# Kernel optimization log

Hardware: AMD Instinct MI355X
Metric: run time of the kernel (lower is better)

Reference implementation:

```python
import jax, jax.numpy as jnp
import numpy as np

B, C, N, M = 128, 1024, 8192, 128  # batch, controller_size, memory_units, key_size(=memory_unit_size)
EPS = 1e-16


def setup_inputs() -> dict:
    key = jax.random.key(0)
    ks = jax.random.split(key, 16)
    controller_state = jax.random.normal(ks[0], (B, C), dtype=jnp.float32)
    pw = jax.random.uniform(ks[1], (B, N), dtype=jnp.float32)
    prev_weights = pw / jnp.sum(pw, axis=1, keepdims=True)  # valid attention distribution
    memory = jax.random.normal(ks[2], (B, N, M), dtype=jnp.float32)
    sc = 0.02
    params = {
        "Wk": sc * jax.random.normal(ks[3], (C, M), dtype=jnp.float32), "bk": jnp.zeros((M,), jnp.float32),
        "Wb": sc * jax.random.normal(ks[4], (C, 1), dtype=jnp.float32), "bb": jnp.zeros((1,), jnp.float32),
        "Wg": sc * jax.random.normal(ks[5], (C, 1), dtype=jnp.float32), "bg": jnp.zeros((1,), jnp.float32),
        "Ws": sc * jax.random.normal(ks[6], (C, 3), dtype=jnp.float32), "bs": jnp.zeros((3,), jnp.float32),
        "Wy": sc * jax.random.normal(ks[7], (C, 1), dtype=jnp.float32), "by": jnp.zeros((1,), jnp.float32),
        "Wa": sc * jax.random.normal(ks[8], (C, M), dtype=jnp.float32), "ba": jnp.zeros((M,), jnp.float32),
    }
    return {"controller_state": controller_state, "prev_weights": prev_weights, "memory": memory, **params}


def reference(controller_state, prev_weights, memory, Wk, bk, Wb, bb, Wg, bg, Ws, bs, Wy, by, Wa, ba):
    cs = controller_state
    k = cs @ Wk + bk                                    # (B, M) key
    beta = jax.nn.softplus(cs @ Wb + bb)                # (B, 1) key strength
    g = jax.nn.sigmoid(cs @ Wg + bg)                    # (B, 1) interpolation gate
    s = jax.nn.softmax(cs @ Ws + bs, axis=1)            # (B, 3) shift weighting
    y = 1.0 + jax.nn.softplus(cs @ Wy + by)             # (B, 1) sharpen factor
    # content addressing: softmax(beta * cosine_sim(key, memory rows))
    dots = jnp.einsum("bnm,bm->bn", memory, k)          # (B, N)
    mnorm = jnp.linalg.norm(memory, axis=2)             # (B, N)
    knorm = jnp.linalg.norm(k, axis=1, keepdims=True)   # (B, 1)
    cos = dots / (mnorm * knorm + EPS)
    content_weights = jax.nn.softmax(beta * cos, axis=1)
    # interpolate with previous weights
    iw = g * content_weights + (1.0 - g) * prev_weights
    # circular 3-tap shift: c[i] = s0*w[i-1] + s1*w[i] + s2*w[i+1] (circular)
    sw = (s[:, 0:1] * jnp.roll(iw, 1, axis=1)
          + s[:, 1:2] * iw
          + s[:, 2:3] * jnp.roll(iw, -1, axis=1))
    # sharpen + normalize
    w = sw ** y
    w = w / (jnp.sum(w, axis=1, keepdims=True) + EPS)
    # read mode: data = w @ memory
    data = jnp.einsum("bn,bnm->bm", w, memory)          # (B, M)
    return (w, data)
```

## Files before the change

kernel.cpp:

```cpp
#include <hip/hip_runtime.h>
#include <math.h>

#define Bsz 128
#define Csz 1024
#define Nsz 8192
#define Msz 128
#define EPSF 1e-16f

__device__ __forceinline__ float softplusf(float x) {
    return (x > 20.f) ? x : log1pf(expf(x));
}

__global__ __launch_bounds__(256) void kA(
    const float* __restrict__ cs,
    const float* __restrict__ Wk, const float* __restrict__ bk,
    const float* __restrict__ Wb, const float* __restrict__ bb,
    const float* __restrict__ Wg, const float* __restrict__ bg,
    const float* __restrict__ Ws, const float* __restrict__ bs,
    const float* __restrict__ Wy, const float* __restrict__ by,
    float* __restrict__ K, float* __restrict__ scal)
{
    const int b = blockIdx.x;
    const int t = threadIdx.x;
    const int m = t & 127, h = t >> 7;
    __shared__ float lcs[Csz];
    __shared__ float kpart[256];
    __shared__ float red[256];

    #pragma unroll
    for (int j = 0; j < Csz / 256; ++j) lcs[t + j * 256] = cs[b * Csz + t + j * 256];
    __syncthreads();

    float ka = 0.f;
    const int c0 = h * (Csz / 2);
    #pragma unroll 8
    for (int c = c0; c < c0 + Csz / 2; ++c) ka += lcs[c] * Wk[c * Msz + m];
    kpart[t] = ka;

    float ab = 0.f, ag = 0.f, ay = 0.f, a0 = 0.f, a1 = 0.f, a2 = 0.f;
    for (int c = t; c < Csz; c += 256) {
        float v = lcs[c];
        ab += v * Wb[c];
        ag += v * Wg[c];
        ay += v * Wy[c];
        a0 += v * Ws[c * 3 + 0];
        a1 += v * Ws[c * 3 + 1];
        a2 += v * Ws[c * 3 + 2];
    }
    __syncthreads();

    float kfull = 0.f;
    if (h == 0) {
        kfull = kpart[m] + kpart[128 + m] + bk[m];
        K[b * Msz + m] = kfull;
    }

    auto redu = [&](float v) -> float {
        __syncthreads();
        red[t] = v;
        __syncthreads();
        for (int off = 128; off > 0; off >>= 1) {
            if (t < off) red[t] += red[t + off];
            __syncthreads();
        }
        return red[0];
    };

    float db = redu(ab);
    float dg = redu(ag);
    float dy = redu(ay);
    float d0 = redu(a0);
    float d1 = redu(a1);
    float d2 = redu(a2);
    float dq = redu(kfull * kfull);

    if (t == 0) {
        float beta = softplusf(db + bb[0]);
        float g = 1.f / (1.f + expf(-(dg + bg[0])));
        float yv = 1.f + softplusf(dy + by[0]);
        float l0 = d0 + bs[0], l1 = d1 + bs[1], l2 = d2 + bs[2];
        float m3 = fmaxf(l0, fmaxf(l1, l2));
        float e0 = expf(l0 - m3), e1 = expf(l1 - m3), e2 = expf(l2 - m3);
        float inv = 1.f / (e0 + e1 + e2);
        scal[b * 8 + 0] = sqrtf(dq);
        scal[b * 8 + 1] = beta;
        scal[b * 8 + 2] = g;
        scal[b * 8 + 3] = e0 * inv;
        scal[b * 8 + 4] = e1 * inv;
        scal[b * 8 + 5] = e2 * inv;
        scal[b * 8 + 6] = yv;
    }
}

__global__ __launch_bounds__(256) void kB(
    const float* __restrict__ mem, const float* __restrict__ K,
    const float* __restrict__ scal, float* __restrict__ z,
    float* __restrict__ sumexp)
{
    const int b = blockIdx.x >> 7;
    const int n0 = (blockIdx.x & 127) * 64;
    const int t = threadIdx.x;
    const int rl = t & 15, rg = t >> 4;

    __shared__ float lk[Msz];
    __shared__ float lred[16];
    if (t < Msz) lk[t] = K[b * Msz + t];
    __syncthreads();

    const float knorm = scal[b * 8 + 0];
    const float beta = scal[b * 8 + 1];

    const float k0 = lk[rl * 4 + 0], k1 = lk[rl * 4 + 1];
    const float k2 = lk[rl * 4 + 2], k3 = lk[rl * 4 + 3];
    const float k4 = lk[64 + rl * 4 + 0], k5 = lk[64 + rl * 4 + 1];
    const float k6 = lk[64 + rl * 4 + 2], k7 = lk[64 + rl * 4 + 3];

    const float* base = mem + (size_t)b * Nsz * Msz;

    float ez = 0.f;
    #pragma unroll
    for (int i = 0; i < 4; ++i) {
        const int n = n0 + i * 16 + rg;
        const float4* p = (const float4*)(base + (size_t)n * Msz);
        float4 a = p[rl];
        float4 c = p[16 + rl];
        float dot = a.x * k0 + a.y * k1 + a.z * k2 + a.w * k3
                  + c.x * k4 + c.y * k5 + c.z * k6 + c.w * k7;
        float sq = a.x * a.x + a.y * a.y + a.z * a.z + a.w * a.w
                 + c.x * c.x + c.y * c.y + c.z * c.z + c.w * c.w;
        #pragma unroll
        for (int off = 8; off; off >>= 1) {
            dot += __shfl_xor(dot, off, 16);
            sq  += __shfl_xor(sq,  off, 16);
        }
        if (rl == 0) {
            float mn = sqrtf(sq);
            float zv = beta * (dot / (mn * knorm + EPSF));
            z[(size_t)b * Nsz + n] = zv;
            ez += expf(zv);
        }
    }
    if (rl == 0) lred[rg] = ez;
    __syncthreads();
    if (t == 0) {
        float s = 0.f;
        #pragma unroll
        for (int j = 0; j < 16; ++j) s += lred[j];
        atomicAdd(&sumexp[b], s);
    }
}

__global__ __launch_bounds__(256) void kD(
    const float* __restrict__ z, const float* __restrict__ pw,
    const float* __restrict__ scal, const float* __restrict__ sumexp,
    float* __restrict__ tbuf, float* __restrict__ S)
{
    const int gid = blockIdx.x * 256 + threadIdx.x;
    const int b = gid >> 13;
    const int n = gid & (Nsz - 1);

    const float invl = 1.f / sumexp[b];
    const float g = scal[b * 8 + 2];
    const float s0 = scal[b * 8 + 3], s1 = scal[b * 8 + 4], s2 = scal[b * 8 + 5];
    const float yv = scal[b * 8 + 6];

    const int nm1 = (n == 0) ? Nsz - 1 : n - 1;
    const int np1 = (n == Nsz - 1) ? 0 : n + 1;
    const size_t bo = (size_t)b * Nsz;

    const float om = 1.f - g;
    float iwm = g * (expf(z[bo + nm1]) * invl) + om * pw[bo + nm1];
    float iw0 = g * (expf(z[bo + n  ]) * invl) + om * pw[bo + n  ];
    float iwp = g * (expf(z[bo + np1]) * invl) + om * pw[bo + np1];

    float sw = s0 * iwm + s1 * iw0 + s2 * iwp;
    float tv = expf(yv * logf(sw));
    tbuf[bo + n] = tv;

    __shared__ float red[256];
    red[threadIdx.x] = tv;
    __syncthreads();
    for (int off = 128; off; off >>= 1) {
        if (threadIdx.x < off) red[threadIdx.x] += red[threadIdx.x + off];
        __syncthreads();
    }
    if (threadIdx.x == 0) atomicAdd(&S[b], red[0]);
}

__global__ __launch_bounds__(256) void kE(
    const float* __restrict__ mem, const float* __restrict__ tbuf,
    const float* __restrict__ S, float* __restrict__ wout,
    float* __restrict__ dacc)
{
    const int ridx = (int)gridDim.x - 1 - (int)blockIdx.x;
    const int b = ridx >> 6;
    const int n0 = (ridx & 63) * 128;
    const int t = threadIdx.x;
    const int rl = t & 15, rg = t >> 4;

    const float invS = 1.f / (S[b] + EPSF);
    const float* base = mem + (size_t)b * Nsz * Msz;
    const float* tb = tbuf + (size_t)b * Nsz;

    float acc[8] = {0.f, 0.f, 0.f, 0.f, 0.f, 0.f, 0.f, 0.f};

    #pragma unroll
    for (int i = 0; i < 8; ++i) {
        const int n = n0 + i * 16 + rg;
        const float tv = tb[n];
        const float4* p = (const float4*)(base + (size_t)n * Msz);
        float4 a = p[rl];
        float4 c = p[16 + rl];
        acc[0] += tv * a.x; acc[1] += tv * a.y; acc[2] += tv * a.z; acc[3] += tv * a.w;
        acc[4] += tv * c.x; acc[5] += tv * c.y; acc[6] += tv * c.z; acc[7] += tv * c.w;
        if (rl == 0) wout[(size_t)b * Nsz + n] = tv * invS;
    }

    __shared__ float red[256 * 8];
    #pragma unroll
    for (int j = 0; j < 8; ++j) red[t * 8 + j] = acc[j];
    __syncthreads();

    if (t < Msz) {
        const int half = t >> 6, rl2 = (t & 63) >> 2, jj = t & 3;
        float s = 0.f;
        #pragma unroll
        for (int gq = 0; gq < 16; ++gq) s += red[(gq * 16 + rl2) * 8 + half * 4 + jj];
        atomicAdd(&dacc[b * Msz + t], s);
    }
}

__global__ __launch_bounds__(256) void kF(
    const float* __restrict__ dacc, const float* __restrict__ S,
    float* __restrict__ dout)
{
    const int gid = blockIdx.x * 256 + threadIdx.x;
    if (gid < Bsz * Msz) {
        const int b = gid >> 7;
        dout[gid] = dacc[gid] / (S[b] + EPSF);
    }
}

extern "C" void kernel_launch(void* const* d_in, const int* in_sizes, int n_in,
                              void* d_out, int out_size, void* d_ws, size_t ws_size,
                              hipStream_t stream) {
    const float* cs  = (const float*)d_in[0];
    const float* pw  = (const float*)d_in[1];
    const float* mem = (const float*)d_in[2];
    const float* Wk  = (const float*)d_in[3];
    const float* bk  = (const float*)d_in[4];
    const float* Wb  = (const float*)d_in[5];
    const float* bb  = (const float*)d_in[6];
    const float* Wg  = (const float*)d_in[7];
    const float* bg  = (const float*)d_in[8];
    const float* Ws  = (const float*)d_in[9];
    const float* bs  = (const float*)d_in[10];
    const float* Wy  = (const float*)d_in[11];
    const float* by  = (const float*)d_in[12];

    float* out = (float*)d_out;
    float* wout = out;
    float* dout = out + (size_t)Bsz * Nsz;

    float* wsf    = (float*)d_ws;
    float* K      = wsf;
    float* scal   = K + Bsz * Msz;
    float* S      = scal + Bsz * 8;
    float* sumexp = S + Bsz;
    float* dacc   = sumexp + Bsz;
    float* z      = dacc + Bsz * Msz;
    float* tbuf   = z + (size_t)Bsz * Nsz;

    hipMemsetAsync(S, 0, (size_t)(Bsz + Bsz + Bsz * Msz) * sizeof(float), stream);

    kA<<<Bsz, 256, 0, stream>>>(cs, Wk, bk, Wb, bb, Wg, bg, Ws, bs, Wy, by, K, scal);
    kB<<<Bsz * (Nsz / 64), 256, 0, stream>>>(mem, K, scal, z, sumexp);
    kD<<<(Bsz * Nsz) / 256, 256, 0, stream>>>(z, pw, scal, sumexp, tbuf, S);
    kE<<<Bsz * (Nsz / 128), 256, 0, stream>>>(mem, tbuf, S, wout, dacc);
    kF<<<(Bsz * Msz + 255) / 256, 256, 0, stream>>>(dacc, S, dout);
}
```

Before: 871.2 us.

## Process batch in chunks so memory re-read hits the last-level cache

Splits the content-addressing, weighting and read kernels into four sequential batch chunks, so the memory slice read by the dot-product kernel is likely still in the large last-level cache when the read kernel touches it again. This targets the second full pass over the large memory tensor from HBM. It adds extra kernel launches and smaller grids per launch, and it replaces the earlier reverse-block-order trick. It also splits the key projection loop into four independent accumulators.

```diff
diff --git a/kernel.cpp b/kernel.cpp
--- a/kernel.cpp
+++ b/kernel.cpp
@@ -6,6 +6,7 @@
 #define Nsz 8192
 #define Msz 128
 #define EPSF 1e-16f
+#define CHUNK 32
 
 __device__ __forceinline__ float softplusf(float x) {
     return (x > 20.f) ? x : log1pf(expf(x));
@@ -31,11 +32,16 @@
     for (int j = 0; j < Csz / 256; ++j) lcs[t + j * 256] = cs[b * Csz + t + j * 256];
     __syncthreads();
 
-    float ka = 0.f;
+    float ka0 = 0.f, ka1 = 0.f, ka2 = 0.f, ka3 = 0.f;
     const int c0 = h * (Csz / 2);
-    #pragma unroll 8
-    for (int c = c0; c < c0 + Csz / 2; ++c) ka += lcs[c] * Wk[c * Msz + m];
-    kpart[t] = ka;
+    #pragma unroll 4
+    for (int c = c0; c < c0 + Csz / 2; c += 4) {
+        ka0 += lcs[c + 0] * Wk[(c + 0) * Msz + m];
+        ka1 += lcs[c + 1] * Wk[(c + 1) * Msz + m];
+        ka2 += lcs[c + 2] * Wk[(c + 2) * Msz + m];
+        ka3 += lcs[c + 3] * Wk[(c + 3) * Msz + m];
+    }
+    kpart[t] = (ka0 + ka1) + (ka2 + ka3);
 
     float ab = 0.f, ag = 0.f, ay = 0.f, a0 = 0.f, a1 = 0.f, a2 = 0.f;
     for (int c = t; c < Csz; c += 256) {
@@ -95,9 +101,9 @@
 __global__ __launch_bounds__(256) void kB(
     const float* __restrict__ mem, const float* __restrict__ K,
     const float* __restrict__ scal, float* __restrict__ z,
-    float* __restrict__ sumexp)
-{
-    const int b = blockIdx.x >> 7;
+    float* __restrict__ sumexp, int b0)
+{
+    const int b = b0 + (blockIdx.x >> 7);
     const int n0 = (blockIdx.x & 127) * 64;
     const int t = threadIdx.x;
     const int rl = t & 15, rg = t >> 4;
@@ -153,10 +159,10 @@
 __global__ __launch_bounds__(256) void kD(
     const float* __restrict__ z, const float* __restrict__ pw,
     const float* __restrict__ scal, const float* __restrict__ sumexp,
-    float* __restrict__ tbuf, float* __restrict__ S)
+    float* __restrict__ tbuf, float* __restrict__ S, int b0)
 {
     const int gid = blockIdx.x * 256 + threadIdx.x;
-    const int b = gid >> 13;
+    const int b = b0 + (gid >> 13);
     const int n = gid & (Nsz - 1);
 
     const float invl = 1.f / sumexp[b];
@@ -190,11 +196,10 @@
 __global__ __launch_bounds__(256) void kE(
     const float* __restrict__ mem, const float* __restrict__ tbuf,
     const float* __restrict__ S, float* __restrict__ wout,
-    float* __restrict__ dacc)
-{
-    const int ridx = (int)gridDim.x - 1 - (int)blockIdx.x;
-    const int b = ridx >> 6;
-    const int n0 = (ridx & 63) * 128;
+    float* __restrict__ dacc, int b0)
+{
+    const int b = b0 + (blockIdx.x >> 6);
+    const int n0 = (blockIdx.x & 63) * 128;
     const int t = threadIdx.x;
     const int rl = t & 15, rg = t >> 4;
 
@@ -274,8 +279,13 @@
     hipMemsetAsync(S, 0, (size_t)(Bsz + Bsz + Bsz * Msz) * sizeof(float), stream);
 
     kA<<<Bsz, 256, 0, stream>>>(cs, Wk, bk, Wb, bb, Wg, bg, Ws, bs, Wy, by, K, scal);
-    kB<<<Bsz * (Nsz / 64), 256, 0, stream>>>(mem, K, scal, z, sumexp);
-    kD<<<(Bsz * Nsz) / 256, 256, 0, stream>>>(z, pw, scal, sumexp, tbuf, S);
-    kE<<<Bsz * (Nsz / 128), 256, 0, stream>>>(mem, tbuf, S, wout, dacc);
+
+    for (int c = Bsz / CHUNK - 1; c >= 0; --c) {
+        const int b0 = c * CHUNK;
+        kB<<<CHUNK * (Nsz / 64), 256, 0, stream>>>(mem, K, scal, z, sumexp, b0);
+        kD<<<(CHUNK * Nsz) / 256, 256, 0, stream>>>(z, pw, scal, sumexp, tbuf, S, b0);
+        kE<<<CHUNK * (Nsz / 128), 256, 0, stream>>>(mem, tbuf, S, wout, dacc, b0);
+    }
+
     kF<<<(Bsz * Msz + 255) / 256, 256, 0, stream>>>(dacc, S, dout);
 }
```

After: 974.5 us. 11.9% more time.
